# Kernel optimization log

Measured on AMD Instinct MI355X. Metric: run time of the kernel, lower is better.

Reference implementation:

```python
import jax, jax.numpy as jnp
import numpy as np

K = 4  # number of processing steps (init kwarg)


def setup_inputs() -> dict:
    key = jax.random.key(0)
    ks = jax.random.split(key, 6)
    B, S, D = 4096, 8192, 512
    H = D  # hidden_size == input_size (residual h + f_x)
    scale = 1.0 / np.sqrt(H)
    return {
        "f_x": jax.random.normal(ks[0], (B, D), dtype=jnp.float32),
        "g_S": jax.random.normal(ks[1], (S, D), dtype=jnp.float32),
        # LSTM step: input f_x (size D), 'hidden' is concat([h, r]) of size 2H
        "W_ih": jax.random.uniform(ks[2], (4 * H, D), jnp.float32, -scale, scale),
        "W_hh": jax.random.uniform(ks[3], (4 * H, 2 * H), jnp.float32, -scale, scale),
        "b_ih": jax.random.uniform(ks[4], (4 * H,), jnp.float32, -scale, scale),
        "b_hh": jax.random.uniform(ks[5], (4 * H,), jnp.float32, -scale, scale),
    }


def _lstm_step(x, hidden, c, W_ih, W_hh, b_ih, b_hh):
    # gates: [B, 4H]; PyTorch LSTMCell gate order (i, f, g, o)
    gates = x @ W_ih.T + b_ih + hidden @ W_hh.T + b_hh
    i, f, g, o = jnp.split(gates, 4, axis=1)
    c_new = jax.nn.sigmoid(f) * c + jax.nn.sigmoid(i) * jnp.tanh(g)
    h_new = jax.nn.sigmoid(o) * jnp.tanh(c_new)
    return h_new, c_new


def reference(f_x, g_S, W_ih, W_hh, b_ih, b_hh):
    # f_x: [B, D] queries; g_S: [S, D] support set embeddings
    h = f_x
    c = jnp.zeros_like(f_x)
    for _ in range(K):
        a = jax.nn.softmax(h @ g_S.T, axis=1)       # [B, S] attention over support
        r = a @ g_S                                  # [B, D] attention readout
        concat = jnp.concatenate([h, r], axis=1)     # [B, 2D]
        h, c = _lstm_step(f_x, concat, c, W_ih, W_hh, b_ih, b_hh)
        h = h + f_x                                  # residual skip connection
    return h
```

## Files before the change

### kernel.cpp

```cpp
#include <hip/hip_runtime.h>

typedef _Float16 f16x8 __attribute__((ext_vector_type(8)));
typedef _Float16 f16x4 __attribute__((ext_vector_type(4)));
typedef float f32x4 __attribute__((ext_vector_type(4)));

#define S_DIM 8192
#define D_DIM 512

__device__ __forceinline__ void gload_lds16(const _Float16* g, _Float16* l) {
  __builtin_amdgcn_global_load_lds(
      (const __attribute__((address_space(1))) unsigned int*)g,
      (__attribute__((address_space(3))) unsigned int*)l, 16, 0, 0);
}

__device__ __forceinline__ float sigf(float x) { return 1.0f / (1.0f + __expf(-x)); }
__device__ __forceinline__ float tanhfast(float x) {
  return 1.0f - 2.0f / (__expf(2.0f * x) + 1.0f);
}


template <int BM, int BN>
__global__ __launch_bounds__(256) void gemm_bt(const _Float16* __restrict__ A, int lda,
                                               const _Float16* __restrict__ B, int ldb,
                                               _Float16* __restrict__ C, int ldc, int K) {
  constexpr int BK = 64;
  constexpr int FM = BM / 32, FN = BN / 32;
  __shared__ _Float16 As[BM * BK];
  __shared__ _Float16 Bs[BN * BK];
  const int tid = threadIdx.x;
  const int lane = tid & 63;
  const int wv = tid >> 6;
  const int bm = blockIdx.y * BM;
  const int bn = blockIdx.x * BN;
  const int wm = (wv >> 1) * (BM / 2);
  const int wn = (wv & 1) * (BN / 2);
  const int fr = lane & 15;
  const int hi4 = lane >> 4;
  const int rx7 = fr & 7;
  const int srow = lane >> 3;
  const int schk = (lane & 7) ^ srow;

  f32x4 acc[FM][FN] = {};

  for (int kt = 0; kt < K; kt += BK) {
    __syncthreads();
#pragma unroll
    for (int p = 0; p < BM / 32; ++p) {
      const int m = wv + 4 * p;
      gload_lds16(A + (size_t)(bm + 8 * m + srow) * lda + kt + schk * 8, As + 512 * m);
    }
#pragma unroll
    for (int p = 0; p < BN / 32; ++p) {
      const int m = wv + 4 * p;
      gload_lds16(B + (size_t)(bn + 8 * m + srow) * ldb + kt + schk * 8, Bs + 512 * m);
    }
    __syncthreads();

#pragma unroll
    for (int h = 0; h < 2; ++h) {
      const int co = (((h << 2) | hi4) ^ rx7) << 3;
      f16x8 af[FM], bf[FN];
#pragma unroll
      for (int i = 0; i < FM; ++i)
        af[i] = *(const f16x8*)&As[(wm + i * 16 + fr) * 64 + co];
#pragma unroll
      for (int j = 0; j < FN; ++j)
        bf[j] = *(const f16x8*)&Bs[(wn + j * 16 + fr) * 64 + co];
#pragma unroll
      for (int i = 0; i < FM; ++i)
#pragma unroll
        for (int j = 0; j < FN; ++j)
          acc[i][j] = __builtin_amdgcn_mfma_f32_16x16x32_f16(af[i], bf[j], acc[i][j], 0, 0, 0);
    }
  }

  const int cc = lane & 15;
  const int cr = (lane >> 4) * 4;
#pragma unroll
  for (int i = 0; i < FM; ++i)
#pragma unroll
    for (int j = 0; j < FN; ++j) {
      size_t base = (size_t)(bm + wm + i * 16 + cr) * ldc + (bn + wn + j * 16 + cc);
#pragma unroll
      for (int r = 0; r < 4; ++r) C[base + (size_t)r * ldc] = (_Float16)acc[i][j][r];
    }
}

__global__ __launch_bounds__(256) void gemm_rsplit(const _Float16* __restrict__ A,
                                                   const _Float16* __restrict__ B,
                                                   _Float16* __restrict__ Pp) {
  constexpr int BK = 64;
  __shared__ _Float16 As[128 * BK];
  __shared__ _Float16 Bs[64 * BK];
  const int tid = threadIdx.x;
  const int lane = tid & 63;
  const int wv = tid >> 6;
  const int bm = blockIdx.x * 128;
  const int bn = blockIdx.y * 64;
  const int kc = blockIdx.z;
  const int k0 = kc * 1024;
  const int wm = (wv >> 1) * 64;
  const int wn = (wv & 1) * 32;
  const int fr = lane & 15;
  const int hi4 = lane >> 4;
  const int rx7 = fr & 7;
  const int srow = lane >> 3;
  const int schk = (lane & 7) ^ srow;

  f32x4 acc[4][2] = {};

  for (int kt = k0; kt < k0 + 1024; kt += BK) {
    __syncthreads();
#pragma unroll
    for (int p = 0; p < 4; ++p) {
      const int m = wv + 4 * p;
      gload_lds16(A + (size_t)(bm + 8 * m + srow) * 8192 + kt + schk * 8, As + 512 * m);
    }
#pragma unroll
    for (int p = 0; p < 2; ++p) {
      const int m = wv + 4 * p;
      gload_lds16(B + (size_t)(bn + 8 * m + srow) * 8192 + kt + schk * 8, Bs + 512 * m);
    }
    __syncthreads();

#pragma unroll
    for (int h = 0; h < 2; ++h) {
      const int co = (((h << 2) | hi4) ^ rx7) << 3;
      f16x8 af[4], bf[2];
#pragma unroll
      for (int i = 0; i < 4; ++i)
        af[i] = *(const f16x8*)&As[(wm + i * 16 + fr) * 64 + co];
#pragma unroll
      for (int j = 0; j < 2; ++j)
        bf[j] = *(const f16x8*)&Bs[(wn + j * 16 + fr) * 64 + co];
#pragma unroll
      for (int i = 0; i < 4; ++i)
#pragma unroll
        for (int j = 0; j < 2; ++j)
          acc[i][j] = __builtin_amdgcn_mfma_f32_16x16x32_f16(af[i], bf[j], acc[i][j], 0, 0, 0);
    }
  }

  const int cc = lane & 15;
  const int cr = (lane >> 4) * 4;
#pragma unroll
  for (int i = 0; i < 4; ++i)
#pragma unroll
    for (int j = 0; j < 2; ++j) {
      size_t base = (size_t)(bm + wm + i * 16 + cr) * 4096 + (size_t)kc * 512 +
                    (bn + wn + j * 16 + cc);
#pragma unroll
      for (int r = 0; r < 4; ++r) Pp[base + (size_t)r * 4096] = (_Float16)acc[i][j][r];
    }
}

__global__ __launch_bounds__(256) void reduce_r(const _Float16* __restrict__ Pp,
                                                _Float16* __restrict__ rout) {
  int idx = blockIdx.x * 256 + threadIdx.x;
  int m = idx >> 7;
  int n4 = (idx & 127) * 4;
  const _Float16* base = Pp + (size_t)m * 4096 + n4;
  f32x4 s = {0.f, 0.f, 0.f, 0.f};
#pragma unroll
  for (int kc = 0; kc < 8; ++kc) {
    f16x4 v = *(const f16x4*)(base + kc * 512);
#pragma unroll
    for (int e = 0; e < 4; ++e) s[e] += (float)v[e];
  }
  f16x4 h = {(_Float16)s[0], (_Float16)s[1], (_Float16)s[2], (_Float16)s[3]};
  *(f16x4*)&rout[(size_t)m * 512 + n4] = h;
}

__global__ __launch_bounds__(256) void gemm_scores_rel(const _Float16* __restrict__ Ah,
                                                       int ldah,
                                                       const _Float16* __restrict__ Al,
                                                       const _Float16* __restrict__ Bh,
                                                       _Float16* __restrict__ P,
                                                       float* __restrict__ M) {
  constexpr int BK = 64;
  __shared__ _Float16 AsH[128 * BK];
  __shared__ _Float16 AsL[128 * BK];
  __shared__ _Float16 BsH[128 * BK];
  __shared__ float rm[2][128];
  const int tid = threadIdx.x;
  const int lane = tid & 63;
  const int wv = tid >> 6;
  const int bm = blockIdx.y * 128;
  const int bn = blockIdx.x * 128;
  const int wm = (wv >> 1) * 64;
  const int wn = (wv & 1) * 64;
  const int fr = lane & 15;
  const int hi4 = lane >> 4;
  const int rx7 = fr & 7;
  const int srow = lane >> 3;
  const int schk = (lane & 7) ^ srow;

  f32x4 acc[4][4] = {};

  for (int kt = 0; kt < 512; kt += BK) {
    __syncthreads();
#pragma unroll
    for (int p = 0; p < 4; ++p) {
      const int m = wv + 4 * p;
      const int row = 8 * m + srow;
      gload_lds16(Ah + (size_t)(bm + row) * ldah + kt + schk * 8, AsH + 512 * m);
      gload_lds16(Al + (size_t)(bm + row) * 512 + kt + schk * 8, AsL + 512 * m);
      gload_lds16(Bh + (size_t)(bn + row) * 512 + kt + schk * 8, BsH + 512 * m);
    }
    __syncthreads();

#pragma unroll
    for (int h = 0; h < 2; ++h) {
      const int co = (((h << 2) | hi4) ^ rx7) << 3;
      f16x8 fah[4], fal[4], fbh[4];
#pragma unroll
      for (int i = 0; i < 4; ++i) {
        fah[i] = *(const f16x8*)&AsH[(wm + i * 16 + fr) * 64 + co];
        fal[i] = *(const f16x8*)&AsL[(wm + i * 16 + fr) * 64 + co];
        fbh[i] = *(const f16x8*)&BsH[(wn + i * 16 + fr) * 64 + co];
      }
#pragma unroll
      for (int i = 0; i < 4; ++i)
#pragma unroll
        for (int j = 0; j < 4; ++j) {
          acc[i][j] = __builtin_amdgcn_mfma_f32_16x16x32_f16(fah[i], fbh[j], acc[i][j], 0, 0, 0);
          acc[i][j] = __builtin_amdgcn_mfma_f32_16x16x32_f16(fal[i], fbh[j], acc[i][j], 0, 0, 0);
        }
    }
  }

  const int cc = lane & 15;
  const int cr = (lane >> 4) * 4;
  float rmax[4][4];
#pragma unroll
  for (int i = 0; i < 4; ++i)
#pragma unroll
    for (int r = 0; r < 4; ++r) {
      float m0 = fmaxf(fmaxf(acc[i][0][r], acc[i][1][r]),
                       fmaxf(acc[i][2][r], acc[i][3][r]));
#pragma unroll
      for (int o = 1; o < 16; o <<= 1) m0 = fmaxf(m0, __shfl_xor(m0, o));
      rmax[i][r] = m0;
    }
  if (cc == 0) {
#pragma unroll
    for (int i = 0; i < 4; ++i)
#pragma unroll
      for (int r = 0; r < 4; ++r) rm[wv & 1][wm + i * 16 + cr + r] = rmax[i][r];
  }
  __syncthreads();
#pragma unroll
  for (int i = 0; i < 4; ++i)
#pragma unroll
    for (int r = 0; r < 4; ++r) {
      const int row = wm + i * 16 + cr + r;
      const float mt = fmaxf(rm[0][row], rm[1][row]);
      if (cc == 0 && (wv & 1) == 0)
        M[(size_t)(bm + row) * 64 + blockIdx.x] = mt;
#pragma unroll
      for (int j = 0; j < 4; ++j)
        P[(size_t)(bm + row) * 8192 + bn + wn + j * 16 + cc] =
            (_Float16)(acc[i][j][r] - mt);
    }
}

__global__ __launch_bounds__(256) void softmax2(_Float16* __restrict__ P,
                                                const float* __restrict__ M) {
  _Float16* p = P + (size_t)blockIdx.x * S_DIM;
  const float* Mr = M + (size_t)blockIdx.x * 64;
  const int tid = threadIdx.x, lane = tid & 63, wave = tid >> 6;
  __shared__ float red[4];
  __shared__ float mt[64];
  if (tid < 64) mt[tid] = Mr[tid];
  __syncthreads();
  float mstar = -3.0e38f;
#pragma unroll 8
  for (int j = 0; j < 64; ++j) mstar = fmaxf(mstar, mt[j]);
  float x[32];
#pragma unroll
  for (int i = 0; i < 4; ++i) {
    f16x8 v = *(const f16x8*)&p[i * 2048 + tid * 8];
    const float off = mt[i * 16 + (tid >> 4)] - mstar;
#pragma unroll
    for (int j = 0; j < 8; ++j) x[i * 8 + j] = (float)v[j] + off;
  }
  float s = 0.f;
#pragma unroll
  for (int k = 0; k < 32; ++k) {
    x[k] = exp2f(x[k] * 1.44269504f);
    s += x[k];
  }
#pragma unroll
  for (int o = 32; o; o >>= 1) s += __shfl_xor(s, o);
  if (lane == 0) red[wave] = s;
  __syncthreads();
  s = (red[0] + red[1]) + (red[2] + red[3]);
  float inv = 1.0f / s;
#pragma unroll
  for (int i = 0; i < 4; ++i) {
    f16x8 v;
#pragma unroll
    for (int j = 0; j < 8; ++j) v[j] = (_Float16)(x[i * 8 + j] * inv);
    *(f16x8*)&p[i * 2048 + tid * 8] = v;
  }
}

__global__ __launch_bounds__(256) void gemm_gates(const _Float16* __restrict__ Ah,
                                                  const _Float16* __restrict__ Ar,
                                                  const _Float16* __restrict__ B,
                                                  const _Float16* __restrict__ gbase,
                                                  const float* __restrict__ bsum,
                                                  const float* __restrict__ f_x,
                                                  float* __restrict__ c,
                                                  _Float16* __restrict__ hnext,
                                                  _Float16* __restrict__ h_lo,
                                                  float* __restrict__ hout) {
  __shared__ _Float16 As[128 * 64];
  __shared__ _Float16 Bs[128 * 64];
  const int tid = threadIdx.x;
  const int lane = tid & 63;
  const int wv = tid >> 6;
  const int n0 = blockIdx.x * 32;
  const int bm = blockIdx.y * 128;
  const int fr = lane & 15;
  const int hi4 = lane >> 4;
  const int rx7 = fr & 7;
  const int srow = lane >> 3;
  const int schk = (lane & 7) ^ srow;

  f32x4 acc[2][8] = {};

  for (int t = 0; t < 16; ++t) {
    const int kt = t * 64;
    __syncthreads();
#pragma unroll
    for (int p = 0; p < 4; ++p) {
      const int m = wv + 4 * p;
      const int arow = bm + 8 * m + srow;
      const _Float16* asrc = (t < 8)
                                 ? Ah + (size_t)arow * 512 + kt + schk * 8
                                 : Ar + (size_t)arow * 512 + (kt - 512) + schk * 8;
      gload_lds16(asrc, As + 512 * m);
      const int brow = 8 * m + srow;
      const int wrow = ((brow >> 5) << 9) + n0 + (brow & 31);
      gload_lds16(B + (size_t)wrow * 1024 + kt + schk * 8, Bs + 512 * m);
    }
    __syncthreads();

#pragma unroll
    for (int h = 0; h < 2; ++h) {
      const int co = (((h << 2) | hi4) ^ rx7) << 3;
      f16x8 af[2], bf[8];
#pragma unroll
      for (int i = 0; i < 2; ++i)
        af[i] = *(const f16x8*)&As[(wv * 32 + i * 16 + fr) * 64 + co];
#pragma unroll
      for (int j = 0; j < 8; ++j)
        bf[j] = *(const f16x8*)&Bs[(j * 16 + fr) * 64 + co];
#pragma unroll
      for (int i = 0; i < 2; ++i)
#pragma unroll
        for (int j = 0; j < 8; ++j)
          acc[i][j] = __builtin_amdgcn_mfma_f32_16x16x32_f16(af[i], bf[j], acc[i][j], 0, 0, 0);
    }
  }

  const int cc = lane & 15;
  const int cr = (lane >> 4) * 4;
#pragma unroll
  for (int jj = 0; jj < 2; ++jj) {
    const int colq = n0 + jj * 16 + cc;
    const float bI = bsum[colq];
    const float bF = bsum[colq + 512];
    const float bG = bsum[colq + 1024];
    const float bO = bsum[colq + 1536];
#pragma unroll
    for (int i = 0; i < 2; ++i)
#pragma unroll
      for (int r = 0; r < 4; ++r) {
        const int row = bm + wv * 32 + i * 16 + cr + r;
        const size_t g0 = (size_t)row * 2048 + colq;
        const float gi = acc[i][jj][r] + (float)gbase[g0] + bI;
        const float gf = acc[i][2 + jj][r] + (float)gbase[g0 + 512] + bF;
        const float gg = acc[i][4 + jj][r] + (float)gbase[g0 + 1024] + bG;
        const float go = acc[i][6 + jj][r] + (float)gbase[g0 + 1536] + bO;
        const size_t o = (size_t)row * 512 + colq;
        const float ci = sigf(gf) * c[o] + sigf(gi) * tanhfast(gg);
        const float hi = sigf(go) * tanhfast(ci) + f_x[o];
        c[o] = ci;
        hout[o] = hi;
        const _Float16 h16 = (_Float16)hi;
        hnext[o] = h16;
        h_lo[o] = (_Float16)(hi - (float)h16);
      }
  }
}

__global__ __launch_bounds__(256) void prep_g(const float* __restrict__ g,
                                              _Float16* __restrict__ gT,
                                              _Float16* __restrict__ g_h) {
  __shared__ _Float16 tile[64][72];
  const int s0 = blockIdx.x * 64;
  const int d0 = blockIdx.y * 64;
  const int t = threadIdx.x;
  const int r = t >> 2;
  const int cq = (t & 3) * 16;
  alignas(16) _Float16 buf[16];
#pragma unroll
  for (int q = 0; q < 4; ++q) {
    f32x4 v = *(const f32x4*)&g[(size_t)(s0 + r) * D_DIM + d0 + cq + q * 4];
#pragma unroll
    for (int e = 0; e < 4; ++e) buf[q * 4 + e] = (_Float16)v[e];
  }
#pragma unroll
  for (int k = 0; k < 16; ++k) tile[r][cq + k] = buf[k];
  *(f16x8*)&g_h[(size_t)(s0 + r) * D_DIM + d0 + cq] = *(const f16x8*)&buf[0];
  *(f16x8*)&g_h[(size_t)(s0 + r) * D_DIM + d0 + cq + 8] = *(const f16x8*)&buf[8];
  __syncthreads();
  alignas(16) _Float16 ob[16];
#pragma unroll
  for (int k = 0; k < 16; ++k) ob[k] = tile[cq + k][r];
  *(f16x8*)&gT[(size_t)(d0 + r) * S_DIM + s0 + cq] = *(const f16x8*)&ob[0];
  *(f16x8*)&gT[(size_t)(d0 + r) * S_DIM + s0 + cq + 8] = *(const f16x8*)&ob[8];
}

__global__ __launch_bounds__(256) void prep_misc(const float* __restrict__ W_ih,
                                                 const float* __restrict__ W_hh,
                                                 const float* __restrict__ f_x,
                                                 const float* __restrict__ b_ih,
                                                 const float* __restrict__ b_hh,
                                                 _Float16* __restrict__ wih_h,
                                                 _Float16* __restrict__ whh_h,
                                                 _Float16* __restrict__ hbufA,
                                                 _Float16* __restrict__ h_lo,
                                                 float* __restrict__ c,
                                                 float* __restrict__ bsum) {
  const int NW1 = 2048 * 512 / 4;
  const int NW2 = 2048 * 1024 / 4;
  const int NFX = 4096 * 512 / 4;
  int idx = blockIdx.x * 256 + threadIdx.x;
  if (idx < NW1) {
    f32x4 v = ((const f32x4*)W_ih)[idx];
    f16x4 h = {(_Float16)v[0], (_Float16)v[1], (_Float16)v[2], (_Float16)v[3]};
    ((f16x4*)wih_h)[idx] = h;
  } else if (idx < NW1 + NW2) {
    int k = idx - NW1;
    f32x4 v = ((const f32x4*)W_hh)[k];
    f16x4 h = {(_Float16)v[0], (_Float16)v[1], (_Float16)v[2], (_Float16)v[3]};
    ((f16x4*)whh_h)[k] = h;
  } else if (idx < NW1 + NW2 + NFX) {
    int k = idx - NW1 - NW2;
    f32x4 v = ((const f32x4*)f_x)[k];
    f16x4 h, lo;
#pragma unroll
    for (int e = 0; e < 4; ++e) {
      h[e] = (_Float16)v[e];
      lo[e] = (_Float16)(v[e] - (float)h[e]);
    }
    ((f16x4*)hbufA)[k] = h;
    ((f16x4*)h_lo)[k] = lo;
    f32x4 z = {0.f, 0.f, 0.f, 0.f};
    ((f32x4*)c)[k] = z;
  } else if (idx < NW1 + NW2 + NFX + 512) {
    int k = idx - NW1 - NW2 - NFX;
    f32x4 bi = ((const f32x4*)b_ih)[k];
    f32x4 bh = ((const f32x4*)b_hh)[k];
    ((f32x4*)bsum)[k] = bi + bh;
  }
}

extern "C" void kernel_launch(void* const* d_in, const int* in_sizes, int n_in,
                              void* d_out, int out_size, void* d_ws, size_t ws_size,
                              hipStream_t stream) {
  const float* f_x = (const float*)d_in[0];
  const float* g_S = (const float*)d_in[1];
  const float* W_ih = (const float*)d_in[2];
  const float* W_hh = (const float*)d_in[3];
  const float* b_ih = (const float*)d_in[4];
  const float* b_hh = (const float*)d_in[5];
  float* hout = (float*)d_out;

  char* w = (char*)d_ws;
  _Float16* P16 = (_Float16*)w;
  _Float16* Pp16 = (_Float16*)(w + 33554432);
  float* Mbuf = (float*)(w + 50331648);
  _Float16* gbase = (_Float16*)(w + 67108864);
  _Float16* hbufA = (_Float16*)(w + 83886080);
  _Float16* hbufB = (_Float16*)(w + 88080384);
  _Float16* g_h = (_Float16*)(w + 92274688);
  _Float16* rbuf = (_Float16*)(w + 100663296);
  float* bsum = (float*)(w + 104857600);
  _Float16* gT = (_Float16*)(w + 109051904);
  _Float16* wih_h = (_Float16*)(w + 117440512);
  _Float16* whh_h = (_Float16*)(w + 119537664);
  float* c = (float*)(w + 123731968);
  _Float16* h_lo = (_Float16*)(w + 132120576);

  prep_g<<<dim3(S_DIM / 64, D_DIM / 64), 256, 0, stream>>>(g_S, gT, g_h);
  prep_misc<<<5122, 256, 0, stream>>>(W_ih, W_hh, f_x, b_ih, b_hh, wih_h, whh_h,
                                      hbufA, h_lo, c, bsum);

  gemm_bt<128, 128><<<dim3(2048 / 128, 4096 / 128), 256, 0, stream>>>(
      hbufA, 512, wih_h, 512, gbase, 2048, 512);

  for (int it = 0; it < 4; ++it) {
    _Float16* hcur = (it & 1) ? hbufB : hbufA;
    _Float16* hnxt = (it & 1) ? hbufA : hbufB;
    for (int hb = 0; hb < 2; ++hb) {
      const _Float16* hhi = hcur + (size_t)hb * 2048 * 512;
      const _Float16* hlo = h_lo + (size_t)hb * 2048 * 512;
      gemm_scores_rel<<<dim3(64, 16), 256, 0, stream>>>(hhi, 512, hlo, g_h, P16, Mbuf);
      softmax2<<<2048, 256, 0, stream>>>(P16, Mbuf);
      gemm_rsplit<<<dim3(16, 8, 8), 256, 0, stream>>>(P16, gT, Pp16);
      reduce_r<<<1024, 256, 0, stream>>>(Pp16, rbuf + (size_t)hb * 2048 * 512);
    }
    gemm_gates<<<dim3(16, 32), 256, 0, stream>>>(hcur, rbuf, whh_h, gbase, bsum,
                                                 f_x, c, hnxt, h_lo, hout);
  }
  (void)in_sizes; (void)n_in; (void)out_size; (void)ws_size;
}
```

Measured before the change: 866.6 us.

## Fuse softmax exponentiation into attention readout GEMM and defer normalization

Removes the separate softmax kernel. The readout GEMM now loads relative scores into registers, applies exp with per-tile max correction, writes the result to LDS, and accumulates per-row partial sums. Normalization by the summed denominators moves into the split-K reduction kernel. The GEMM tile also widens from 128x64 to 128x128 to improve reuse, and the partial outputs now sit in the second half of an enlarged P row stride. Together this avoids a full read and write pass over the B×S probability matrix, at the cost of more registers and exp work inside the GEMM loop.

```diff
diff --git a/kernel.cpp b/kernel.cpp
--- a/kernel.cpp
+++ b/kernel.cpp
@@ -86,58 +86,113 @@
     }
 }
 
-__global__ __launch_bounds__(256) void gemm_rsplit(const _Float16* __restrict__ A,
-                                                   const _Float16* __restrict__ B,
-                                                   _Float16* __restrict__ Pp) {
-  constexpr int BK = 64;
-  __shared__ _Float16 As[128 * BK];
-  __shared__ _Float16 Bs[64 * BK];
+__global__ __launch_bounds__(256) void gemm_rsplit_exp(const _Float16* __restrict__ P,
+                                                       const _Float16* __restrict__ B,
+                                                       const float* __restrict__ M,
+                                                       _Float16* __restrict__ Pp,
+                                                       float* __restrict__ Sg) {
+  __shared__ _Float16 As[128 * 64];
+  __shared__ _Float16 Bs[128 * 64];
+  __shared__ float Ms[128][8];
+  __shared__ float msh[128];
   const int tid = threadIdx.x;
   const int lane = tid & 63;
   const int wv = tid >> 6;
   const int bm = blockIdx.x * 128;
-  const int bn = blockIdx.y * 64;
+  const int bn = blockIdx.y * 128;
   const int kc = blockIdx.z;
   const int k0 = kc * 1024;
   const int wm = (wv >> 1) * 64;
-  const int wn = (wv & 1) * 32;
+  const int wn = (wv & 1) * 64;
   const int fr = lane & 15;
   const int hi4 = lane >> 4;
   const int rx7 = fr & 7;
   const int srow = lane >> 3;
-  const int schk = (lane & 7) ^ srow;
-
-  f32x4 acc[4][2] = {};
-
-  for (int kt = k0; kt < k0 + 1024; kt += BK) {
-    __syncthreads();
+  const int achk = lane & 7;
+  const int schk = achk ^ srow;
+  constexpr float L2E = 1.44269504f;
+
+  if (tid < 128) {
+    const float* Mr = M + (size_t)(bm + tid) * 64;
+    float mm = -3.0e38f;
+#pragma unroll
+    for (int q = 0; q < 16; ++q) {
+      f32x4 v = ((const f32x4*)Mr)[q];
+      mm = fmaxf(mm, fmaxf(fmaxf(v[0], v[1]), fmaxf(v[2], v[3])));
+    }
+    msh[tid] = mm;
+#pragma unroll
+    for (int j = 0; j < 8; ++j) Ms[tid][j] = Mr[kc * 8 + j];
+  }
+
+  f32x4 acc[4][4] = {};
+  float psum[4] = {0.f, 0.f, 0.f, 0.f};
+  f16x8 areg[4];
+
+  auto load_a = [&](int kt) {
 #pragma unroll
     for (int p = 0; p < 4; ++p) {
       const int m = wv + 4 * p;
-      gload_lds16(A + (size_t)(bm + 8 * m + srow) * 8192 + kt + schk * 8, As + 512 * m);
-    }
-#pragma unroll
-    for (int p = 0; p < 2; ++p) {
+      areg[p] = *(const f16x8*)(P + (size_t)(bm + 8 * m + srow) * 16384 + kt + achk * 8);
+    }
+  };
+
+  __syncthreads();
+  load_a(k0);
+
+  for (int kt = k0; kt < k0 + 1024; kt += 64) {
+    __syncthreads();
+    const int nbk = (kt - k0) >> 7;
+#pragma unroll
+    for (int p = 0; p < 4; ++p) {
+      const int m = wv + 4 * p;
+      const int row = 8 * m + srow;
+      const float off = (Ms[row][nbk] - msh[row]) * L2E;
+      f16x8 o;
+      float ps = 0.f;
+#pragma unroll
+      for (int e = 0; e < 8; ++e) {
+        float x = exp2f(fmaf((float)areg[p][e], L2E, off));
+        ps += x;
+        o[e] = (_Float16)x;
+      }
+      psum[p] += ps;
+      *(f16x8*)&As[512 * m + srow * 64 + (achk ^ srow) * 8] = o;
+    }
+#pragma unroll
+    for (int p = 0; p < 4; ++p) {
       const int m = wv + 4 * p;
       gload_lds16(B + (size_t)(bn + 8 * m + srow) * 8192 + kt + schk * 8, Bs + 512 * m);
     }
     __syncthreads();
+    if (kt + 64 < k0 + 1024) load_a(kt + 64);
 
 #pragma unroll
     for (int h = 0; h < 2; ++h) {
       const int co = (((h << 2) | hi4) ^ rx7) << 3;
-      f16x8 af[4], bf[2];
+      f16x8 af[4], bf[4];
+#pragma unroll
+      for (int i = 0; i < 4; ++i) {
+        af[i] = *(const f16x8*)&As[(wm + i * 16 + fr) * 64 + co];
+        bf[i] = *(const f16x8*)&Bs[(wn + i * 16 + fr) * 64 + co];
+      }
 #pragma unroll
       for (int i = 0; i < 4; ++i)
-        af[i] = *(const f16x8*)&As[(wm + i * 16 + fr) * 64 + co];
-#pragma unroll
-      for (int j = 0; j < 2; ++j)
-        bf[j] = *(const f16x8*)&Bs[(wn + j * 16 + fr) * 64 + co];
-#pragma unroll
-      for (int i = 0; i < 4; ++i)
-#pragma unroll
-        for (int j = 0; j < 2; ++j)
+#pragma unroll
+        for (int j = 0; j < 4; ++j)
           acc[i][j] = __builtin_amdgcn_mfma_f32_16x16x32_f16(af[i], bf[j], acc[i][j], 0, 0, 0);
+    }
+  }
+
+  if (blockIdx.y == 0) {
+#pragma unroll
+    for (int p = 0; p < 4; ++p) {
+      float s = psum[p];
+      s += __shfl_xor(s, 1);
+      s += __shfl_xor(s, 2);
+      s += __shfl_xor(s, 4);
+      if ((lane & 7) == 0)
+        Sg[(size_t)(bm + 8 * (wv + 4 * p) + srow) * 8 + kc] = s;
     }
   }
 
@@ -146,20 +201,24 @@
 #pragma unroll
   for (int i = 0; i < 4; ++i)
 #pragma unroll
-    for (int j = 0; j < 2; ++j) {
-      size_t base = (size_t)(bm + wm + i * 16 + cr) * 4096 + (size_t)kc * 512 +
+    for (int j = 0; j < 4; ++j) {
+      size_t base = (size_t)(bm + wm + i * 16 + cr) * 16384 + 8192 + (size_t)kc * 512 +
                     (bn + wn + j * 16 + cc);
 #pragma unroll
-      for (int r = 0; r < 4; ++r) Pp[base + (size_t)r * 4096] = (_Float16)acc[i][j][r];
+      for (int r = 0; r < 4; ++r) Pp[base + (size_t)r * 16384] = (_Float16)acc[i][j][r];
     }
 }
 
 __global__ __launch_bounds__(256) void reduce_r(const _Float16* __restrict__ Pp,
+                                                const float* __restrict__ Sg,
                                                 _Float16* __restrict__ rout) {
   int idx = blockIdx.x * 256 + threadIdx.x;
   int m = idx >> 7;
   int n4 = (idx & 127) * 4;
-  const _Float16* base = Pp + (size_t)m * 4096 + n4;
+  f32x4 s0 = ((const f32x4*)(Sg + (size_t)m * 8))[0];
+  f32x4 s1 = ((const f32x4*)(Sg + (size_t)m * 8))[1];
+  float inv = 1.0f / ((s0[0] + s0[1] + s0[2] + s0[3]) + (s1[0] + s1[1] + s1[2] + s1[3]));
+  const _Float16* base = Pp + (size_t)m * 16384 + 8192 + n4;
   f32x4 s = {0.f, 0.f, 0.f, 0.f};
 #pragma unroll
   for (int kc = 0; kc < 8; ++kc) {
@@ -167,7 +226,8 @@
 #pragma unroll
     for (int e = 0; e < 4; ++e) s[e] += (float)v[e];
   }
-  f16x4 h = {(_Float16)s[0], (_Float16)s[1], (_Float16)s[2], (_Float16)s[3]};
+  f16x4 h = {(_Float16)(s[0] * inv), (_Float16)(s[1] * inv), (_Float16)(s[2] * inv),
+             (_Float16)(s[3] * inv)};
   *(f16x4*)&rout[(size_t)m * 512 + n4] = h;
 }
 
@@ -259,50 +319,9 @@
         M[(size_t)(bm + row) * 64 + blockIdx.x] = mt;
 #pragma unroll
       for (int j = 0; j < 4; ++j)
-        P[(size_t)(bm + row) * 8192 + bn + wn + j * 16 + cc] =
+        P[(size_t)(bm + row) * 16384 + bn + wn + j * 16 + cc] =
             (_Float16)(acc[i][j][r] - mt);
     }
-}
-
-__global__ __launch_bounds__(256) void softmax2(_Float16* __restrict__ P,
-                                                const float* __restrict__ M) {
-  _Float16* p = P + (size_t)blockIdx.x * S_DIM;
-  const float* Mr = M + (size_t)blockIdx.x * 64;
-  const int tid = threadIdx.x, lane = tid & 63, wave = tid >> 6;
-  __shared__ float red[4];
-  __shared__ float mt[64];
-  if (tid < 64) mt[tid] = Mr[tid];
-  __syncthreads();
-  float mstar = -3.0e38f;
-#pragma unroll 8
-  for (int j = 0; j < 64; ++j) mstar = fmaxf(mstar, mt[j]);
-  float x[32];
-#pragma unroll
-  for (int i = 0; i < 4; ++i) {
-    f16x8 v = *(const f16x8*)&p[i * 2048 + tid * 8];
-    const float off = mt[i * 16 + (tid >> 4)] - mstar;
-#pragma unroll
-    for (int j = 0; j < 8; ++j) x[i * 8 + j] = (float)v[j] + off;
-  }
-  float s = 0.f;
-#pragma unroll
-  for (int k = 0; k < 32; ++k) {
-    x[k] = exp2f(x[k] * 1.44269504f);
-    s += x[k];
-  }
-#pragma unroll
-  for (int o = 32; o; o >>= 1) s += __shfl_xor(s, o);
-  if (lane == 0) red[wave] = s;
-  __syncthreads();
-  s = (red[0] + red[1]) + (red[2] + red[3]);
-  float inv = 1.0f / s;
-#pragma unroll
-  for (int i = 0; i < 4; ++i) {
-    f16x8 v;
-#pragma unroll
-    for (int j = 0; j < 8; ++j) v[j] = (_Float16)(x[i * 8 + j] * inv);
-    *(f16x8*)&p[i * 2048 + tid * 8] = v;
-  }
 }
 
 __global__ __launch_bounds__(256) void gemm_gates(const _Float16* __restrict__ Ah,
@@ -482,14 +501,14 @@
 
   char* w = (char*)d_ws;
   _Float16* P16 = (_Float16*)w;
-  _Float16* Pp16 = (_Float16*)(w + 33554432);
-  float* Mbuf = (float*)(w + 50331648);
   _Float16* gbase = (_Float16*)(w + 67108864);
   _Float16* hbufA = (_Float16*)(w + 83886080);
   _Float16* hbufB = (_Float16*)(w + 88080384);
   _Float16* g_h = (_Float16*)(w + 92274688);
   _Float16* rbuf = (_Float16*)(w + 100663296);
   float* bsum = (float*)(w + 104857600);
+  float* Sg = (float*)(w + 104865792);
+  float* Mbuf = (float*)(w + 104931328);
   _Float16* gT = (_Float16*)(w + 109051904);
   _Float16* wih_h = (_Float16*)(w + 117440512);
   _Float16* whh_h = (_Float16*)(w + 119537664);
@@ -510,9 +529,8 @@
       const _Float16* hhi = hcur + (size_t)hb * 2048 * 512;
       const _Float16* hlo = h_lo + (size_t)hb * 2048 * 512;
       gemm_scores_rel<<<dim3(64, 16), 256, 0, stream>>>(hhi, 512, hlo, g_h, P16, Mbuf);
-      softmax2<<<2048, 256, 0, stream>>>(P16, Mbuf);
-      gemm_rsplit<<<dim3(16, 8, 8), 256, 0, stream>>>(P16, gT, Pp16);
-      reduce_r<<<1024, 256, 0, stream>>>(Pp16, rbuf + (size_t)hb * 2048 * 512);
+      gemm_rsplit_exp<<<dim3(16, 4, 8), 256, 0, stream>>>(P16, gT, Mbuf, P16, Sg);
+      reduce_r<<<1024, 256, 0, stream>>>(P16, Sg, rbuf + (size_t)hb * 2048 * 512);
     }
     gemm_gates<<<dim3(16, 32), 256, 0, stream>>>(hcur, rbuf, whh_h, gbase, bsum,
                                                  f_x, c, hnxt, h_lo, hout);
```

Measured after the change: 873.2 us. Within noise of the previous version (+0.8%).
